# Kernel optimization log

Hardware: AMD Instinct MI355X
Metric: run time of the kernel (lower is better)

The kernel has to match this reference:

```python
import jax, jax.numpy as jnp
import numpy as np

SCALE = 1.0 / np.sqrt(128.0).astype(np.float32)  # 1/sqrt(head_dim)


def setup_inputs() -> dict:
    key = jax.random.key(0)
    kq, kk, kv = jax.random.split(key, 3)
    B, S, D = 32, 2048, 128
    q = jax.random.normal(kq, (B, S, D), dtype=jnp.float32)
    k = jax.random.normal(kk, (B, S, D), dtype=jnp.float32)
    v = jax.random.normal(kv, (B, S, D), dtype=jnp.float32)
    return {"q": q, "k": k, "v": v}


def reference(q, k, v):
    # attention = bmm(q, k^T) * scale ; softmax over last (key) dim; bmm with v
    scores = jnp.einsum("bsd,btd->bst", q, k) * SCALE  # [B, S, S]
    attn = jax.nn.softmax(scores, axis=-1)
    return jnp.einsum("bst,btd->bsd", attn, v)  # [B, S, D]
```

## Files before the change

kernel.cpp:

```cpp
#include <hip/hip_runtime.h>
#include <math.h>
#include <stdint.h>

typedef __bf16 bf16_t;
typedef __bf16 bf16x2 __attribute__((ext_vector_type(2)));
typedef __bf16 bf16x4 __attribute__((ext_vector_type(4)));
typedef __bf16 bf16x8 __attribute__((ext_vector_type(8)));
typedef float f32x4 __attribute__((ext_vector_type(4)));
typedef float f32x16 __attribute__((ext_vector_type(16)));

#define NB   32
#define SEQ  2048
#define HD   128
#define SCALE 0.08838834764831845f
#define LOG2E 1.4426950408889634f

__device__ __forceinline__ float fast_exp2(float x) {
#if __has_builtin(__builtin_amdgcn_exp2f)
  return __builtin_amdgcn_exp2f(x);
#else
  return exp2f(x);
#endif
}

__global__ __launch_bounds__(256) void prep_kernel(
    const float* __restrict__ Q, const float* __restrict__ K,
    const float* __restrict__ V, bf16_t* __restrict__ Qs,
    bf16_t* __restrict__ Kb, bf16_t* __restrict__ Vt)
{
  const int b = blockIdx.x;
  const int tid = threadIdx.x;
  if (b < 4096) {
    const bool isQ = (b < 2048);
    const float* src = isQ ? Q : K;
    bf16_t* dst = isQ ? Qs : Kb;
    const float sc = isQ ? (SCALE * LOG2E) : 1.0f;
    size_t base4 = (size_t)(isQ ? b : b - 2048) * 1024;
#pragma unroll
    for (int i = 0; i < 4; ++i) {
      size_t idx = base4 + tid + i * 256;
      float4 x = ((const float4*)src)[idx];
      bf16x4 y;
      y[0] = (bf16_t)(x.x * sc); y[1] = (bf16_t)(x.y * sc);
      y[2] = (bf16_t)(x.z * sc); y[3] = (bf16_t)(x.w * sc);
      ((bf16x4*)dst)[idx] = y;
    }
  } else {
    __shared__ float tile[64][65];
    const int bt = b - 4096;
    const int batch = bt >> 6;
    const int rem = bt & 63;
    const int s0 = (rem >> 1) * 64;
    const int d0 = (rem & 1) * 64;
#pragma unroll
    for (int i = 0; i < 4; ++i) {
      int e = tid + i * 256;
      int s = e >> 4, dq = e & 15;
      float4 x = *(const float4*)&V[((size_t)batch * SEQ + s0 + s) * HD + d0 + dq * 4];
      tile[s][dq * 4 + 0] = x.x;
      tile[s][dq * 4 + 1] = x.y;
      tile[s][dq * 4 + 2] = x.z;
      tile[s][dq * 4 + 3] = x.w;
    }
    __syncthreads();
#pragma unroll
    for (int i = 0; i < 2; ++i) {
      int g = tid + i * 256;
      int d = g >> 3, sg = g & 7;
      bf16x8 w;
#pragma unroll
      for (int j = 0; j < 8; ++j) w[j] = (bf16_t)tile[sg * 8 + j][d];
      *(bf16x8*)&Vt[((size_t)batch * HD + d0 + d) * SEQ + s0 + sg * 8] = w;
    }
  }
}

__global__ __launch_bounds__(256) void fa14_kernel(
    const bf16_t* __restrict__ Qs, const bf16_t* __restrict__ Kbf,
    const bf16_t* __restrict__ Vt, float* __restrict__ O)
{
  __shared__ __attribute__((aligned(16))) char smem[81920];
  bf16_t* const Ksw = (bf16_t*)smem;
  bf16_t* const Vsw = (bf16_t*)(smem + 32768);

  const int tid  = threadIdx.x;
  const int lane = tid & 63;
  const int wq   = tid >> 6;
  const int hi   = lane >> 5;
  const int q31  = lane & 31;
  const int pair = wq >> 1;
  const int sub  = wq & 1;
  const int koff = sub * 32;

  const int L     = ((blockIdx.x & 7) << 7) | (blockIdx.x >> 3);
  const int batch = L >> 5;
  const int qt    = L & 31;

  const bf16_t* Qb = Qs + ((size_t)batch * SEQ + qt * 64 + pair * 32) * HD;
  const bf16_t* Kb = Kbf + (size_t)batch * SEQ * HD;
  const bf16_t* Vb = Vt + (size_t)batch * HD * SEQ;
  float*        Ob = O + ((size_t)batch * SEQ + qt * 64) * HD;

  bf16x8 bq[8];
#pragma unroll
  for (int dc = 0; dc < 8; ++dc)
    bq[dc] = *(const bf16x8*)&Qb[(size_t)q31 * HD + dc * 16 + hi * 8];

  f32x16 o[4];
#pragma unroll
  for (int dt = 0; dt < 4; ++dt)
#pragma unroll
    for (int r = 0; r < 16; ++r) o[dt][r] = 0.f;
  float m_r = -INFINITY, l_r = 0.0f;

  bf16x8 bp0p, bp1p;

  auto stage = [&](int kbuf, int vbuf, int kb) {
#pragma unroll
    for (int i = 0; i < 4; ++i) {
      int row = wq * 16 + i * 4 + (lane >> 4);
      int gk = (lane & 15) ^ (row & 15);
      const bf16_t* gp = Kb + (size_t)(kb + row) * HD + gk * 8;
      __builtin_amdgcn_global_load_lds(
          (const __attribute__((address_space(1))) void*)gp,
          (__attribute__((address_space(3))) void*)&Ksw[kbuf * 8192 + (wq * 16 + i * 4) * 128],
          16, 0, 0);
    }
#pragma unroll
    for (int i = 0; i < 4; ++i) {
      int d = wq * 32 + i * 8 + (lane >> 3);
      int gv = (lane & 7) ^ (d & 7);
      const bf16_t* gp = Vb + (size_t)d * SEQ + kb + gv * 8;
      __builtin_amdgcn_global_load_lds(
          (const __attribute__((address_space(1))) void*)gp,
          (__attribute__((address_space(3))) void*)&Vsw[vbuf * 8192 + (wq * 32 + i * 8) * 64],
          16, 0, 0);
    }
  };

  stage(0, 0, 0);

  for (int t = 0; t < SEQ / 64; ++t) {
    __syncthreads();
    const int vnext = (t + 1) % 3;
    const int vprev = (t + 2) % 3;
    if (t + 1 < SEQ / 64) stage((t + 1) & 1, vnext, (t + 1) * 64);

    const bf16_t* Ks = &Ksw[(t & 1) * 8192];

    f32x16 s;
#pragma unroll
    for (int r = 0; r < 16; ++r) s[r] = 0.f;
    {
      const int row = koff + q31;
      const int rsw = row & 15;
#pragma unroll
      for (int dc = 0; dc < 8; ++dc) {
        bf16x8 ak = *(const bf16x8*)&Ks[row * 128 + (((dc * 2 + hi) ^ rsw) * 8)];
        s = __builtin_amdgcn_mfma_f32_32x32x16_bf16(ak, bq[dc], s, 0, 0, 0);
      }
    }

    if (t > 0) {
      const bf16_t* Vp = &Vsw[vprev * 8192];
      const int g0 = (koff >> 3) + hi;
      const int g1 = g0 + 2;
#pragma unroll
      for (int dt = 0; dt < 4; ++dt) {
        const int d = dt * 32 + q31;
        const int dsw = d & 7;
        bf16x8 av0 = *(const bf16x8*)&Vp[d * 64 + ((g0 ^ dsw) * 8)];
        o[dt] = __builtin_amdgcn_mfma_f32_32x32x16_bf16(av0, bp0p, o[dt], 0, 0, 0);
        bf16x8 av1 = *(const bf16x8*)&Vp[d * 64 + ((g1 ^ dsw) * 8)];
        o[dt] = __builtin_amdgcn_mfma_f32_32x32x16_bf16(av1, bp1p, o[dt], 0, 0, 0);
      }
    }

    float mx = s[0];
#pragma unroll
    for (int r = 1; r < 16; ++r) mx = fmaxf(mx, s[r]);
    mx = fmaxf(mx, __shfl_xor(mx, 32));

    if (!__all(mx <= m_r + 8.0f)) {
      const float mnew = fmaxf(m_r, mx);
      const float alpha = fast_exp2(m_r - mnew);
      m_r = mnew;
      l_r *= alpha;
#pragma unroll
      for (int dt = 0; dt < 4; ++dt) o[dt] = o[dt] * alpha;
    }

    float ls = 0.f;
#pragma unroll
    for (int r = 0; r < 16; ++r) {
      float p = fast_exp2(s[r] - m_r);
      s[r] = p; ls += p;
    }
    ls += __shfl_xor(ls, 32);
    l_r += ls;

    uint32_t pk[8];
#pragma unroll
    for (int i = 0; i < 8; ++i) {
      union { bf16x2 v; uint32_t u; } c;
      c.v[0] = (bf16_t)s[2 * i];
      c.v[1] = (bf16_t)s[2 * i + 1];
      pk[i] = c.u;
    }
    uint32_t t0 = __shfl_xor((int)(hi ? pk[0] : pk[2]), 32);
    uint32_t t1 = __shfl_xor((int)(hi ? pk[1] : pk[3]), 32);
    uint32_t t2 = __shfl_xor((int)(hi ? pk[4] : pk[6]), 32);
    uint32_t t3 = __shfl_xor((int)(hi ? pk[5] : pk[7]), 32);
    {
      union { bf16x8 v; uint32_t w[4]; } B;
      if (hi) { B.w[0] = t0; B.w[1] = t1; B.w[2] = pk[2]; B.w[3] = pk[3]; }
      else    { B.w[0] = pk[0]; B.w[1] = pk[1]; B.w[2] = t0; B.w[3] = t1; }
      bp0p = B.v;
      if (hi) { B.w[0] = t2; B.w[1] = t3; B.w[2] = pk[6]; B.w[3] = pk[7]; }
      else    { B.w[0] = pk[4]; B.w[1] = pk[5]; B.w[2] = t2; B.w[3] = t3; }
      bp1p = B.v;
    }
  }

  {
    const bf16_t* Vp = &Vsw[((SEQ / 64 - 1) % 3) * 8192];
    const int g0 = (koff >> 3) + hi;
    const int g1 = g0 + 2;
#pragma unroll
    for (int dt = 0; dt < 4; ++dt) {
      const int d = dt * 32 + q31;
      const int dsw = d & 7;
      bf16x8 av0 = *(const bf16x8*)&Vp[d * 64 + ((g0 ^ dsw) * 8)];
      o[dt] = __builtin_amdgcn_mfma_f32_32x32x16_bf16(av0, bp0p, o[dt], 0, 0, 0);
      bf16x8 av1 = *(const bf16x8*)&Vp[d * 64 + ((g1 ^ dsw) * 8)];
      o[dt] = __builtin_amdgcn_mfma_f32_32x32x16_bf16(av1, bp1p, o[dt], 0, 0, 0);
    }
  }

  __syncthreads();
  float* const sf  = (float*)smem;
  float* const mlb = (float*)(smem + 33792);

  if (sub == 1) {
    if (hi == 0) {
      mlb[pair * 64 + q31]      = m_r;
      mlb[pair * 64 + 32 + q31] = l_r;
    }
#pragma unroll
    for (int dt = 0; dt < 4; ++dt)
#pragma unroll
      for (int r = 0; r < 16; ++r) {
        int d = dt * 32 + (r & 3) + 8 * (r >> 2) + 4 * hi;
        sf[pair * 4224 + q31 * 132 + d] = o[dt][r];
      }
  }
  __syncthreads();
  if (sub == 0) {
    float m1 = mlb[pair * 64 + q31];
    float l1 = mlb[pair * 64 + 32 + q31];
    float m = fmaxf(m_r, m1);
    float e0 = fast_exp2(m_r - m);
    float e1 = fast_exp2(m1 - m);
    float inv = 1.0f / (l_r * e0 + l1 * e1);
    float f0 = e0 * inv, f1 = e1 * inv;
#pragma unroll
    for (int dt = 0; dt < 4; ++dt)
#pragma unroll
      for (int r = 0; r < 16; ++r) {
        int d = dt * 32 + (r & 3) + 8 * (r >> 2) + 4 * hi;
        float* p = &sf[pair * 4224 + q31 * 132 + d];
        *p = o[dt][r] * f0 + *p * f1;
      }
  }
  __syncthreads();
  {
    const int tid2 = sub * 64 + lane;
#pragma unroll
    for (int i = 0; i < 8; ++i) {
      int idx = tid2 + i * 128;
      int q = idx >> 5;
      int dg = idx & 31;
      float4 v = *(const float4*)&sf[pair * 4224 + q * 132 + dg * 4];
      *(float4*)&Ob[(size_t)(pair * 32 + q) * HD + dg * 4] = v;
    }
  }
}

#define BM   64
#define BN   64
#define KPAD 8
#define VPAD 8
#define PPAD 8

__global__ __launch_bounds__(256) void fa_fallback(
    const float* __restrict__ Q, const float* __restrict__ K,
    const float* __restrict__ V, float* __restrict__ O)
{
  __shared__ __attribute__((aligned(16))) bf16_t Ksh[BN][HD + KPAD];
  __shared__ __attribute__((aligned(16))) bf16_t Vsh[HD][BN + VPAD];
  __shared__ __attribute__((aligned(16))) bf16_t Psh[4][16][BN + PPAD];

  const int tid = threadIdx.x;
  const int lane = tid & 63;
  const int wq = tid >> 6;
  const int quad = lane >> 4;
  const int l15 = lane & 15;
  const int bid = blockIdx.x;
  const int batch = bid >> 5;
  const int qt = bid & 31;

  const float* Qb = Q + (size_t)batch * SEQ * HD + (size_t)qt * BM * HD;
  const float* Kb = K + (size_t)batch * SEQ * HD;
  const float* Vb = V + (size_t)batch * SEQ * HD;
  float* Ob = O + (size_t)batch * SEQ * HD + (size_t)qt * BM * HD;

  bf16x8 aq[4];
  {
    const int qrow = wq * 16 + l15;
#pragma unroll
    for (int kf = 0; kf < 4; ++kf) {
      const float* qp = Qb + (size_t)qrow * HD + kf * 32 + quad * 8;
      float4 x0 = *(const float4*)(qp);
      float4 x1 = *(const float4*)(qp + 4);
      bf16x8 a;
      a[0] = (bf16_t)(x0.x * SCALE); a[1] = (bf16_t)(x0.y * SCALE);
      a[2] = (bf16_t)(x0.z * SCALE); a[3] = (bf16_t)(x0.w * SCALE);
      a[4] = (bf16_t)(x1.x * SCALE); a[5] = (bf16_t)(x1.y * SCALE);
      a[6] = (bf16_t)(x1.z * SCALE); a[7] = (bf16_t)(x1.w * SCALE);
      aq[kf] = a;
    }
  }

  f32x4 o[8];
#pragma unroll
  for (int t = 0; t < 8; ++t) { o[t][0]=0.f; o[t][1]=0.f; o[t][2]=0.f; o[t][3]=0.f; }
  float m_r = -INFINITY, l_r = 0.0f;
  const int vkp = (tid & 31) * 2;
  const int vg = tid >> 5;
  float4 kreg[8], vreg[8];

#pragma unroll
  for (int i = 0; i < 8; ++i) {
    int v = tid + i * 256, row = v >> 5, c4 = (v & 31) * 4;
    kreg[i] = *(const float4*)(Kb + (size_t)row * HD + c4);
  }
#pragma unroll
  for (int i = 0; i < 4; ++i) {
    int d0 = (vg + i * 8) * 4;
    const float* vp0 = Vb + (size_t)vkp * HD + d0;
    vreg[2 * i] = *(const float4*)vp0;
    vreg[2 * i + 1] = *(const float4*)(vp0 + HD);
  }

  for (int kb = 0; kb < SEQ; kb += BN) {
    __syncthreads();
#pragma unroll
    for (int i = 0; i < 8; ++i) {
      int v = tid + i * 256, row = v >> 5, c4 = (v & 31) * 4;
      float4 kv = kreg[i];
      bf16x4 kk;
      kk[0]=(bf16_t)kv.x; kk[1]=(bf16_t)kv.y; kk[2]=(bf16_t)kv.z; kk[3]=(bf16_t)kv.w;
      *(bf16x4*)&Ksh[row][c4] = kk;
    }
#pragma unroll
    for (int i = 0; i < 4; ++i) {
      int d0 = (vg + i * 8) * 4;
      float4 a0 = vreg[2 * i], a1 = vreg[2 * i + 1];
      bf16x2 p0; p0[0]=(bf16_t)a0.x; p0[1]=(bf16_t)a1.x;
      bf16x2 p1; p1[0]=(bf16_t)a0.y; p1[1]=(bf16_t)a1.y;
      bf16x2 p2; p2[0]=(bf16_t)a0.z; p2[1]=(bf16_t)a1.z;
      bf16x2 p3; p3[0]=(bf16_t)a0.w; p3[1]=(bf16_t)a1.w;
      *(bf16x2*)&Vsh[d0 + 0][vkp] = p0;
      *(bf16x2*)&Vsh[d0 + 1][vkp] = p1;
      *(bf16x2*)&Vsh[d0 + 2][vkp] = p2;
      *(bf16x2*)&Vsh[d0 + 3][vkp] = p3;
    }
    __syncthreads();

    const int kbn = kb + BN;
    if (kbn < SEQ) {
#pragma unroll
      for (int i = 0; i < 8; ++i) {
        int v = tid + i * 256, row = v >> 5, c4 = (v & 31) * 4;
        kreg[i] = *(const float4*)(Kb + (size_t)(kbn + row) * HD + c4);
      }
#pragma unroll
      for (int i = 0; i < 4; ++i) {
        int d0 = (vg + i * 8) * 4;
        const float* vp0 = Vb + (size_t)(kbn + vkp) * HD + d0;
        vreg[2 * i] = *(const float4*)vp0;
        vreg[2 * i + 1] = *(const float4*)(vp0 + HD);
      }
    }

    f32x4 s[4];
#pragma unroll
    for (int ct = 0; ct < 4; ++ct) { s[ct][0]=0.f; s[ct][1]=0.f; s[ct][2]=0.f; s[ct][3]=0.f; }
#pragma unroll
    for (int kf = 0; kf < 4; ++kf)
#pragma unroll
      for (int ct = 0; ct < 4; ++ct) {
        bf16x8 ak = *(const bf16x8*)&Ksh[ct * 16 + l15][kf * 32 + quad * 8];
        s[ct] = __builtin_amdgcn_mfma_f32_16x16x32_bf16(ak, aq[kf], s[ct], 0, 0, 0);
      }

    float mx = s[0][0];
#pragma unroll
    for (int ct = 0; ct < 4; ++ct)
#pragma unroll
      for (int r = 0; r < 4; ++r) mx = fmaxf(mx, s[ct][r]);
    mx = fmaxf(mx, __shfl_xor(mx, 16));
    mx = fmaxf(mx, __shfl_xor(mx, 32));
    float mnew = fmaxf(m_r, mx);
    float alpha = __expf(m_r - mnew);
    m_r = mnew;
    float ls = 0.f;
#pragma unroll
    for (int ct = 0; ct < 4; ++ct)
#pragma unroll
      for (int r = 0; r < 4; ++r) {
        float p = __expf(s[ct][r] - mnew);
        s[ct][r] = p; ls += p;
      }
    ls += __shfl_xor(ls, 16);
    ls += __shfl_xor(ls, 32);
    l_r = l_r * alpha + ls;

#pragma unroll
    for (int ct = 0; ct < 4; ++ct) {
      bf16x4 pp;
      pp[0]=(bf16_t)s[ct][0]; pp[1]=(bf16_t)s[ct][1];
      pp[2]=(bf16_t)s[ct][2]; pp[3]=(bf16_t)s[ct][3];
      *(bf16x4*)&Psh[wq][l15][ct * 16 + quad * 4] = pp;
    }
    asm volatile("s_waitcnt lgkmcnt(0)" ::: "memory");
    bf16x8 ap0 = *(const bf16x8*)&Psh[wq][l15][quad * 8];
    bf16x8 ap1 = *(const bf16x8*)&Psh[wq][l15][32 + quad * 8];

#pragma unroll
    for (int t = 0; t < 8; ++t) {
      o[t][0]*=alpha; o[t][1]*=alpha; o[t][2]*=alpha; o[t][3]*=alpha;
    }
#pragma unroll
    for (int t = 0; t < 8; ++t) {
      bf16x8 av0 = *(const bf16x8*)&Vsh[t * 16 + l15][quad * 8];
      o[t] = __builtin_amdgcn_mfma_f32_16x16x32_bf16(av0, ap0, o[t], 0, 0, 0);
      bf16x8 av1 = *(const bf16x8*)&Vsh[t * 16 + l15][32 + quad * 8];
      o[t] = __builtin_amdgcn_mfma_f32_16x16x32_bf16(av1, ap1, o[t], 0, 0, 0);
    }
  }

  float inv = 1.0f / l_r;
  const int qrow = wq * 16 + l15;
#pragma unroll
  for (int t = 0; t < 8; ++t) {
    float4 w;
    w.x = o[t][0]*inv; w.y = o[t][1]*inv; w.z = o[t][2]*inv; w.w = o[t][3]*inv;
    *(float4*)&Ob[(size_t)qrow * HD + t * 16 + quad * 4] = w;
  }
}

extern "C" void kernel_launch(void* const* d_in, const int* in_sizes, int n_in,
                              void* d_out, int out_size, void* d_ws, size_t ws_size,
                              hipStream_t stream) {
  const float* q = (const float*)d_in[0];
  const float* k = (const float*)d_in[1];
  const float* v = (const float*)d_in[2];
  float* out = (float*)d_out;

  const size_t elems = (size_t)NB * SEQ * HD;
  const size_t need = elems * 2 * 3;

  if (ws_size >= need) {
    bf16_t* Qs = (bf16_t*)d_ws;
    bf16_t* Kb = Qs + elems;
    bf16_t* Vt = Kb + elems;
    prep_kernel<<<6144, 256, 0, stream>>>(q, k, v, Qs, Kb, Vt);
    fa14_kernel<<<NB * (SEQ / 64), 256, 0, stream>>>(Qs, Kb, Vt, out);
  } else {
    fa_fallback<<<NB * (SEQ / BM), 256, 0, stream>>>(q, k, v, out);
  }
}
```

Baseline: 232.3 us.

## Fuse Q conversion into attention kernel, add MFMA priority hints, tree-reduce row max

Removes the Q fp32-to-bf16 pre-pass from the prep kernel. The attention kernel now loads fp32 Q directly and applies the scale and bf16 conversion in registers, which cuts a full write and read of a bf16 Q copy plus a third of the prep work. It also raises wave priority around the MFMA sections with s_setprio, and replaces the serial row-max chain with a balanced tree. The trade-off is that each attention block reads fp32 Q with wider loads and does a little extra conversion work at kernel start.

Result: faster. 225.0 us (-3.1%).

```diff
diff --git a/kernel.cpp b/kernel.cpp
--- a/kernel.cpp
+++ b/kernel.cpp
@@ -24,30 +24,25 @@
 }
 
 __global__ __launch_bounds__(256) void prep_kernel(
-    const float* __restrict__ Q, const float* __restrict__ K,
-    const float* __restrict__ V, bf16_t* __restrict__ Qs,
+    const float* __restrict__ K, const float* __restrict__ V,
     bf16_t* __restrict__ Kb, bf16_t* __restrict__ Vt)
 {
   const int b = blockIdx.x;
   const int tid = threadIdx.x;
-  if (b < 4096) {
-    const bool isQ = (b < 2048);
-    const float* src = isQ ? Q : K;
-    bf16_t* dst = isQ ? Qs : Kb;
-    const float sc = isQ ? (SCALE * LOG2E) : 1.0f;
-    size_t base4 = (size_t)(isQ ? b : b - 2048) * 1024;
+  if (b < 2048) {
+    size_t base4 = (size_t)b * 1024;
 #pragma unroll
     for (int i = 0; i < 4; ++i) {
       size_t idx = base4 + tid + i * 256;
-      float4 x = ((const float4*)src)[idx];
+      float4 x = ((const float4*)K)[idx];
       bf16x4 y;
-      y[0] = (bf16_t)(x.x * sc); y[1] = (bf16_t)(x.y * sc);
-      y[2] = (bf16_t)(x.z * sc); y[3] = (bf16_t)(x.w * sc);
-      ((bf16x4*)dst)[idx] = y;
+      y[0] = (bf16_t)x.x; y[1] = (bf16_t)x.y;
+      y[2] = (bf16_t)x.z; y[3] = (bf16_t)x.w;
+      ((bf16x4*)Kb)[idx] = y;
     }
   } else {
     __shared__ float tile[64][65];
-    const int bt = b - 4096;
+    const int bt = b - 2048;
     const int batch = bt >> 6;
     const int rem = bt & 63;
     const int s0 = (rem >> 1) * 64;
@@ -75,8 +70,8 @@
   }
 }
 
-__global__ __launch_bounds__(256) void fa14_kernel(
-    const bf16_t* __restrict__ Qs, const bf16_t* __restrict__ Kbf,
+__global__ __launch_bounds__(256) void fa15_kernel(
+    const float* __restrict__ Q, const bf16_t* __restrict__ Kbf,
     const bf16_t* __restrict__ Vt, float* __restrict__ O)
 {
   __shared__ __attribute__((aligned(16))) char smem[81920];
@@ -96,15 +91,27 @@
   const int batch = L >> 5;
   const int qt    = L & 31;
 
-  const bf16_t* Qb = Qs + ((size_t)batch * SEQ + qt * 64 + pair * 32) * HD;
+  const float*  Qb = Q   + ((size_t)batch * SEQ + qt * 64 + pair * 32) * HD;
   const bf16_t* Kb = Kbf + (size_t)batch * SEQ * HD;
-  const bf16_t* Vb = Vt + (size_t)batch * HD * SEQ;
-  float*        Ob = O + ((size_t)batch * SEQ + qt * 64) * HD;
+  const bf16_t* Vb = Vt  + (size_t)batch * HD * SEQ;
+  float*        Ob = O   + ((size_t)batch * SEQ + qt * 64) * HD;
 
   bf16x8 bq[8];
-#pragma unroll
-  for (int dc = 0; dc < 8; ++dc)
-    bq[dc] = *(const bf16x8*)&Qb[(size_t)q31 * HD + dc * 16 + hi * 8];
+  {
+    const float qs = SCALE * LOG2E;
+#pragma unroll
+    for (int dc = 0; dc < 8; ++dc) {
+      const float* qp = Qb + (size_t)q31 * HD + dc * 16 + hi * 8;
+      float4 x0 = *(const float4*)qp;
+      float4 x1 = *(const float4*)(qp + 4);
+      bf16x8 a;
+      a[0] = (bf16_t)(x0.x * qs); a[1] = (bf16_t)(x0.y * qs);
+      a[2] = (bf16_t)(x0.z * qs); a[3] = (bf16_t)(x0.w * qs);
+      a[4] = (bf16_t)(x1.x * qs); a[5] = (bf16_t)(x1.y * qs);
+      a[6] = (bf16_t)(x1.z * qs); a[7] = (bf16_t)(x1.w * qs);
+      bq[dc] = a;
+    }
+  }
 
   f32x16 o[4];
 #pragma unroll
@@ -148,6 +155,8 @@
 
     const bf16_t* Ks = &Ksw[(t & 1) * 8192];
 
+    __builtin_amdgcn_s_setprio(1);
+
     f32x16 s;
 #pragma unroll
     for (int r = 0; r < 16; ++r) s[r] = 0.f;
@@ -175,10 +184,13 @@
         o[dt] = __builtin_amdgcn_mfma_f32_32x32x16_bf16(av1, bp1p, o[dt], 0, 0, 0);
       }
     }
-
-    float mx = s[0];
-#pragma unroll
-    for (int r = 1; r < 16; ++r) mx = fmaxf(mx, s[r]);
+    __builtin_amdgcn_s_setprio(0);
+
+    float ma = fmaxf(fmaxf(s[0],  s[1]),  fmaxf(s[2],  s[3]));
+    float mb = fmaxf(fmaxf(s[4],  s[5]),  fmaxf(s[6],  s[7]));
+    float mc = fmaxf(fmaxf(s[8],  s[9]),  fmaxf(s[10], s[11]));
+    float md = fmaxf(fmaxf(s[12], s[13]), fmaxf(s[14], s[15]));
+    float mx = fmaxf(fmaxf(ma, mb), fmaxf(mc, md));
     mx = fmaxf(mx, __shfl_xor(mx, 32));
 
     if (!__all(mx <= m_r + 8.0f)) {
@@ -226,6 +238,7 @@
     const bf16_t* Vp = &Vsw[((SEQ / 64 - 1) % 3) * 8192];
     const int g0 = (koff >> 3) + hi;
     const int g1 = g0 + 2;
+    __builtin_amdgcn_s_setprio(1);
 #pragma unroll
     for (int dt = 0; dt < 4; ++dt) {
       const int d = dt * 32 + q31;
@@ -235,6 +248,7 @@
       bf16x8 av1 = *(const bf16x8*)&Vp[d * 64 + ((g1 ^ dsw) * 8)];
       o[dt] = __builtin_amdgcn_mfma_f32_32x32x16_bf16(av1, bp1p, o[dt], 0, 0, 0);
     }
+    __builtin_amdgcn_s_setprio(0);
   }
 
   __syncthreads();
@@ -469,14 +483,13 @@
   float* out = (float*)d_out;
 
   const size_t elems = (size_t)NB * SEQ * HD;
-  const size_t need = elems * 2 * 3;
+  const size_t need = elems * 2 * 2;
 
   if (ws_size >= need) {
-    bf16_t* Qs = (bf16_t*)d_ws;
-    bf16_t* Kb = Qs + elems;
+    bf16_t* Kb = (bf16_t*)d_ws;
     bf16_t* Vt = Kb + elems;
-    prep_kernel<<<6144, 256, 0, stream>>>(q, k, v, Qs, Kb, Vt);
-    fa14_kernel<<<NB * (SEQ / 64), 256, 0, stream>>>(Qs, Kb, Vt, out);
+    prep_kernel<<<4096, 256, 0, stream>>>(k, v, Kb, Vt);
+    fa15_kernel<<<NB * (SEQ / 64), 256, 0, stream>>>(q, Kb, Vt, out);
   } else {
     fa_fallback<<<NB * (SEQ / BM), 256, 0, stream>>>(q, k, v, out);
   }
```
